# Performance work log

Hardware: AMD Instinct MI355X
Metric: run time of the kernel (lower is better)

The kernel has to match this reference:

```python
import jax, jax.numpy as jnp
import numpy as np
import math

D_MODEL, N_HEADS, D_K, D_V = 512, 2, 64, 64
C_CLIP = 10.0
MASK_FILL = -10.0

def setup_inputs() -> dict:
    key = jax.random.key(0)
    ks = jax.random.split(key, 12)
    B, Lq, Lk = 4, 2048, 2048
    s = 1.0 / math.sqrt(D_MODEL)
    return {
        "Q": jax.random.normal(ks[0], (B, Lq, D_MODEL), jnp.float32),
        "K": jax.random.normal(ks[1], (B, Lk, D_MODEL), jnp.float32),
        "V": jax.random.normal(ks[2], (B, Lk, D_MODEL), jnp.float32),
        "mask": jax.random.randint(ks[3], (B, Lk), 0, 2) > 0,
        "Wq": jax.random.normal(ks[4], (D_MODEL, N_HEADS * D_K), jnp.float32) * s,
        "bq": jnp.zeros((N_HEADS * D_K,), jnp.float32),
        "Wk": jax.random.normal(ks[5], (D_MODEL, N_HEADS * D_K), jnp.float32) * s,
        "bk": jnp.zeros((N_HEADS * D_K,), jnp.float32),
        "Wv": jax.random.normal(ks[6], (D_MODEL, N_HEADS * D_V), jnp.float32) * s,
        "bv": jnp.zeros((N_HEADS * D_V,), jnp.float32),
        "Wo": jax.random.normal(ks[7], (N_HEADS * D_V, D_MODEL), jnp.float32) * s,
        "bo": jnp.zeros((D_MODEL,), jnp.float32),
    }

def reference(Q, K, V, mask, Wq, bq, Wk, bk, Wv, bv, Wo, bo):
    B, Lq, _ = Q.shape
    Lk = K.shape[1]
    # project and split heads: [B, h, L, d]
    q = (Q @ Wq + bq).reshape(B, Lq, N_HEADS, D_K).transpose(0, 2, 1, 3)
    k = (K @ Wk + bk).reshape(B, Lk, N_HEADS, D_K).transpose(0, 2, 1, 3)
    v = (V @ Wv + bv).reshape(B, Lk, N_HEADS, D_V).transpose(0, 2, 1, 3)
    scores = jnp.einsum("bhqd,bhkd->bhqk", q, k) / jnp.sqrt(jnp.float32(D_K))
    scores = jnp.tanh(scores) * C_CLIP
    scores = jnp.where(mask[:, None, None, :], MASK_FILL, scores)
    attn = jax.nn.log_softmax(scores, axis=-1)  # NOTE: log-softmax used directly as weights
    out = jnp.einsum("bhqk,bhkd->bhqd", attn, v)
    out = out.transpose(0, 2, 1, 3).reshape(B, Lq, N_HEADS * D_V)
    out = out @ Wo + bo
    return (out, attn)
```

## Files before the change

kernel.cpp:

```cpp
#include <hip/hip_runtime.h>

typedef __attribute__((ext_vector_type(8))) short short8;
typedef __attribute__((ext_vector_type(4))) float f32x4;

#define DEVI static __device__ __forceinline__

constexpr int NB   = 4;
constexpr int NH   = 2;
constexpr int SEQ  = 2048;
constexpr int DM   = 512;
constexpr int DKV  = 64;
constexpr int HDIM = 128;

DEVI unsigned short f2bf(float f) {
    union { float f; unsigned u; } v; v.f = f;
    unsigned r = v.u + 0x7FFFu + ((v.u >> 16) & 1u);
    return (unsigned short)(r >> 16);
}
DEVI float bf2f(unsigned short s) {
    union { unsigned u; float f; } v; v.u = ((unsigned)s) << 16; return v.f;
}
DEVI void async16(const void* g, void* l) {
    __builtin_amdgcn_global_load_lds(
        (const __attribute__((address_space(1))) unsigned int*)g,
        (__attribute__((address_space(3))) unsigned int*)l, 16, 0, 0);
}

__global__ __launch_bounds__(256) void k_prep(
    const float* __restrict__ Wq, const float* __restrict__ Wk,
    const float* __restrict__ Wv, const float* __restrict__ Wo,
    unsigned short* __restrict__ Wqt, unsigned short* __restrict__ Wkt,
    unsigned short* __restrict__ Wvt, unsigned short* __restrict__ Wot) {
    int id = blockIdx.x * 256 + threadIdx.x;
    int which = id >> 16;
    int rem = id & 65535;
    if (which < 3) {
        const float* W = which == 0 ? Wq : (which == 1 ? Wk : Wv);
        unsigned short* Wt = which == 0 ? Wqt : (which == 1 ? Wkt : Wvt);
        int n = rem >> 9, k = rem & 511;
        Wt[rem] = f2bf(W[k * HDIM + n]);
    } else {
        int n = rem >> 7, k = rem & 127;
        Wot[rem] = f2bf(Wo[k * DM + n]);
    }
}

__global__ __launch_bounds__(256) void k_proj(
    const float* __restrict__ Qg, const float* __restrict__ Kg, const float* __restrict__ Vg,
    const unsigned short* __restrict__ Wqt, const unsigned short* __restrict__ Wkt,
    const unsigned short* __restrict__ Wvt,
    const float* __restrict__ bq, const float* __restrict__ bk, const float* __restrict__ bv,
    unsigned short* __restrict__ qs, unsigned short* __restrict__ kb,
    unsigned short* __restrict__ vt) {
    __shared__ unsigned short lA[64 * 64];
    __shared__ unsigned short lB[128 * 64];

    const int y = blockIdx.y;
    const float* X = y == 0 ? Qg : (y == 1 ? Kg : Vg);
    const unsigned short* Wt = y == 0 ? Wqt : (y == 1 ? Wkt : Wvt);
    const float* bias = y == 0 ? bq : (y == 1 ? bk : bv);
    const float scal = y == 0 ? 0.125f : 1.0f;
    const int row0 = blockIdx.x * 64;
    const int tid = threadIdx.x, lane = tid & 63, wv = tid >> 6;
    const int l16 = lane & 15, lq4 = lane >> 4;
    const int wr = wv >> 1, wc = wv & 1;

    f32x4 acc[2][4];
    #pragma unroll
    for (int i = 0; i < 2; ++i)
        #pragma unroll
        for (int j = 0; j < 4; ++j) acc[i][j] = f32x4{0.f, 0.f, 0.f, 0.f};

    const int arow = tid >> 2, ac0 = (tid & 3) * 16;

    for (int kc = 0; kc < 8; ++kc) {
        {
            const float* src = X + (size_t)(row0 + arow) * DM + kc * 64 + ac0;
            #pragma unroll
            for (int i = 0; i < 4; ++i) {
                float4 v = *(const float4*)(src + 4 * i);
                unsigned p0 = (unsigned)f2bf(v.x) | ((unsigned)f2bf(v.y) << 16);
                unsigned p1 = (unsigned)f2bf(v.z) | ((unsigned)f2bf(v.w) << 16);
                int slot = ((tid & 3) * 2 + (i >> 1)) ^ (arow & 7);
                char* d = (char*)lA + arow * 128 + slot * 16 + (i & 1) * 8;
                *(unsigned*)d = p0;
                *(unsigned*)(d + 4) = p1;
            }
        }
        #pragma unroll
        for (int c = 0; c < 4; ++c) {
            int chunk = wv * 4 + c;
            int n = chunk * 8 + (lane >> 3);
            int gslot = (lane & 7) ^ (n & 7);
            const void* g = (const char*)Wt + ((size_t)n * DM + kc * 64) * 2 + gslot * 16;
            void* l = (char*)lB + chunk * 1024 + lane * 16;
            async16(g, l);
        }
        __syncthreads();

        #pragma unroll
        for (int ks = 0; ks < 2; ++ks) {
            short8 a[2], b[4];
            #pragma unroll
            for (int mt = 0; mt < 2; ++mt) {
                int m = wr * 32 + mt * 16 + l16;
                unsigned ao = (unsigned)(m * 128 + ks * 64 + lq4 * 16) ^ ((unsigned)(m & 7) << 4);
                a[mt] = *(const short8*)((const char*)lA + ao);
            }
            #pragma unroll
            for (int nt = 0; nt < 4; ++nt) {
                int n = wc * 64 + nt * 16 + l16;
                unsigned bo2 = (unsigned)(n * 128 + ks * 64 + lq4 * 16) ^ ((unsigned)(n & 7) << 4);
                b[nt] = *(const short8*)((const char*)lB + bo2);
            }
            #pragma unroll
            for (int mt = 0; mt < 2; ++mt)
                #pragma unroll
                for (int nt = 0; nt < 4; ++nt)
                    acc[mt][nt] = __builtin_amdgcn_mfma_f32_16x16x32_bf16(
                        a[mt], b[nt], acc[mt][nt], 0, 0, 0);
        }
        __syncthreads();
    }

    if (y < 2) {
        unsigned short* dstp = (y == 0) ? qs : kb;
        #pragma unroll
        for (int mt = 0; mt < 2; ++mt)
            #pragma unroll
            for (int nt = 0; nt < 4; ++nt) {
                int col = wc * 64 + nt * 16 + l16;
                float bb = bias[col];
                int h = col >> 6, d = col & 63;
                #pragma unroll
                for (int r = 0; r < 4; ++r) {
                    int row = row0 + wr * 32 + mt * 16 + lq4 * 4 + r;
                    int b = row >> 11, pos = row & 2047;
                    float val = (acc[mt][nt][r] + bb) * scal;
                    dstp[((size_t)(b * NH + h) * SEQ + pos) * DKV + d] = f2bf(val);
                }
            }
    } else {
        #pragma unroll
        for (int mt = 0; mt < 2; ++mt)
            #pragma unroll
            for (int nt = 0; nt < 4; ++nt) {
                int col = wc * 64 + nt * 16 + l16;
                float bb = bias[col];
                #pragma unroll
                for (int r = 0; r < 4; ++r) {
                    int mrow = wr * 32 + mt * 16 + lq4 * 4 + r;
                    lB[col * 64 + mrow] = f2bf(acc[mt][nt][r] + bb);
                }
            }
        __syncthreads();
        int c = tid >> 1, mp = (tid & 1) * 32;
        int b = row0 >> 11, kpos0 = row0 & 2047;
        int h = c >> 6, d = c & 63;
        unsigned short* dst = vt + ((size_t)(b * NH + h) * DKV + d) * SEQ + kpos0 + mp;
        const unsigned short* srcl = &lB[c * 64 + mp];
        #pragma unroll
        for (int i = 0; i < 4; ++i)
            *(uint4*)(dst + 8 * i) = *(const uint4*)(srcl + 8 * i);
    }
}

__global__ __launch_bounds__(512) void k_fused(
    const unsigned short* __restrict__ qs, const unsigned short* __restrict__ kb,
    const unsigned short* __restrict__ vt, const int* __restrict__ maskg,
    float* __restrict__ attnG, unsigned short* __restrict__ outh) {
    __shared__ unsigned short sAttn[32 * 2048];
    __shared__ float lsum[4][32];
    __shared__ float lL[32];

    const int wg = blockIdx.x;
    const int swz = (wg & 7) * 64 + (wg >> 3);
    const int bh = swz >> 6;
    const int qt = swz & 63;
    const int qbase = qt * 32;
    const int b = bh >> 1, h = bh & 1;
    const int tid = threadIdx.x, lane = tid & 63, wv = tid >> 6;
    const int l16 = lane & 15, lq4 = lane >> 4;
    const int wr = wv >> 2, wc = wv & 3;

    const unsigned short* qrow =
        qs + ((size_t)bh * SEQ + qbase + wr * 16 + l16) * DKV + lq4 * 8;
    short8 aq0 = *(const short8*)qrow;
    short8 aq1 = *(const short8*)(qrow + 32);

    const unsigned short* kfrag =
        kb + ((size_t)bh * SEQ + wc * 16 + l16) * DKV + lq4 * 8;
    const int* mrow = maskg + b * SEQ + wc * 16 + l16;

    const int srow_q = wr * 16 + lq4 * 4;
    const int cbase = wc * 16 + l16;

    float sums[4] = {0.f, 0.f, 0.f, 0.f};

    #pragma unroll 2
    for (int kt = 0; kt < 32; ++kt) {
        short8 b0 = *(const short8*)(kfrag + (size_t)kt * 4096);
        short8 b1 = *(const short8*)(kfrag + (size_t)kt * 4096 + 32);
        int mv = mrow[kt * 64];
        f32x4 acc = f32x4{0.f, 0.f, 0.f, 0.f};
        acc = __builtin_amdgcn_mfma_f32_16x16x32_bf16(aq0, b0, acc, 0, 0, 0);
        acc = __builtin_amdgcn_mfma_f32_16x16x32_bf16(aq1, b1, acc, 0, 0, 0);
        int col = kt * 64 + cbase;
        #pragma unroll
        for (int r = 0; r < 4; ++r) {
            float x = acc[r];
            float e2 = __expf(2.f * x);
            float s10 = 10.f - 20.f * __builtin_amdgcn_rcpf(1.f + e2);
            float s = mv ? -10.f : s10;
            sums[r] += __expf(s);
            int row = srow_q + r;
            unsigned bo = (unsigned)(row * 4096 + col * 2) ^ ((unsigned)(row & 7) << 4);
            *(unsigned short*)((char*)sAttn + bo) = f2bf(s);
        }
    }

    #pragma unroll
    for (int r = 0; r < 4; ++r) {
        float v = sums[r];
        v += __shfl_xor(v, 1); v += __shfl_xor(v, 2);
        v += __shfl_xor(v, 4); v += __shfl_xor(v, 8);
        if (l16 == 0) lsum[wc][srow_q + r] = v;
    }
    __syncthreads();
    if (tid < 32)
        lL[tid] = __logf(lsum[0][tid] + lsum[1][tid] + lsum[2][tid] + lsum[3][tid]);
    __syncthreads();

    {
        const int row = tid >> 4;
        const int cb = (tid & 15) * 8;
        const float Lv = lL[row];
        float* gdst = attnG + ((size_t)bh * SEQ + qbase + row) * SEQ;
        const unsigned rbase = (unsigned)(row * 4096);
        const unsigned rxor = (unsigned)(row & 7) << 4;
        #pragma unroll
        for (int j = 0; j < 16; ++j) {
            int c = cb + j * 128;
            unsigned bo = (rbase + (unsigned)(c * 2)) ^ rxor;
            short8 v = *(const short8*)((const char*)sAttn + bo);
            float fv[8];
            #pragma unroll
            for (int t = 0; t < 8; ++t) fv[t] = bf2f((unsigned short)v[t]) - Lv;
            float4 fa, fb;
            fa.x = fv[0]; fa.y = fv[1]; fa.z = fv[2]; fa.w = fv[3];
            fb.x = fv[4]; fb.y = fv[5]; fb.z = fv[6]; fb.w = fv[7];
            *(float4*)(gdst + c) = fa;
            *(float4*)(gdst + c + 4) = fb;
            short8 w;
            #pragma unroll
            for (int t = 0; t < 8; ++t) w[t] = (short)f2bf(fv[t]);
            *(short8*)((char*)sAttn + bo) = w;
        }
    }
    __syncthreads();

    const unsigned short* vfrag =
        vt + ((size_t)bh * DKV + wc * 16 + l16) * SEQ + lq4 * 8;
    const int arow = wr * 16 + l16;
    const unsigned abase = (unsigned)(arow * 4096);
    const unsigned axor = (unsigned)(arow & 7) << 4;
    f32x4 o = f32x4{0.f, 0.f, 0.f, 0.f};
    #pragma unroll 4
    for (int ks = 0; ks < 64; ++ks) {
        short8 af = *(const short8*)((const char*)sAttn +
                                     ((abase + (unsigned)(ks * 64 + lq4 * 16)) ^ axor));
        short8 vf = *(const short8*)(vfrag + ks * 32);
        o = __builtin_amdgcn_mfma_f32_16x16x32_bf16(af, vf, o, 0, 0, 0);
    }

    #pragma unroll
    for (int r = 0; r < 4; ++r) {
        size_t orow = (size_t)b * SEQ + qbase + wr * 16 + lq4 * 4 + r;
        outh[orow * HDIM + h * DKV + wc * 16 + l16] = f2bf(o[r]);
    }
}

__global__ __launch_bounds__(256) void k_oproj(
    const unsigned short* __restrict__ outh, const unsigned short* __restrict__ Wot,
    const float* __restrict__ bo, float* __restrict__ outG) {
    __shared__ unsigned short lA2[128 * 128];
    __shared__ unsigned short lB2[128 * 128];
    const int row0 = blockIdx.x * 128, col0 = blockIdx.y * 128;
    const int tid = threadIdx.x, lane = tid & 63, wv = tid >> 6;
    const int l16 = lane & 15, lq4 = lane >> 4;
    const int wr = wv >> 1, wc = wv & 1;

    #pragma unroll
    for (int c = 0; c < 8; ++c) {
        int chunk = wv * 8 + c;
        int row = chunk * 4 + (lane >> 4);
        int gslot = (lane & 15) ^ (row & 7);
        async16((const char*)outh + ((size_t)(row0 + row)) * 256 + gslot * 16,
                (char*)lA2 + chunk * 1024 + lane * 16);
    }
    #pragma unroll
    for (int c = 0; c < 8; ++c) {
        int chunk = wv * 8 + c;
        int row = chunk * 4 + (lane >> 4);
        int gslot = (lane & 15) ^ (row & 7);
        async16((const char*)Wot + ((size_t)(col0 + row)) * 256 + gslot * 16,
                (char*)lB2 + chunk * 1024 + lane * 16);
    }
    __syncthreads();

    f32x4 acc[4][4];
    #pragma unroll
    for (int mt = 0; mt < 4; ++mt)
        #pragma unroll
        for (int nt = 0; nt < 4; ++nt) acc[mt][nt] = f32x4{0.f, 0.f, 0.f, 0.f};

    #pragma unroll
    for (int ks = 0; ks < 4; ++ks) {
        short8 a[4], bfr[4];
        #pragma unroll
        for (int mt = 0; mt < 4; ++mt) {
            int m = wr * 64 + mt * 16 + l16;
            unsigned ao = (unsigned)(m * 256 + ks * 64 + lq4 * 16) ^ ((unsigned)(m & 7) << 4);
            a[mt] = *(const short8*)((const char*)lA2 + ao);
        }
        #pragma unroll
        for (int nt = 0; nt < 4; ++nt) {
            int n = wc * 64 + nt * 16 + l16;
            unsigned bo2 = (unsigned)(n * 256 + ks * 64 + lq4 * 16) ^ ((unsigned)(n & 7) << 4);
            bfr[nt] = *(const short8*)((const char*)lB2 + bo2);
        }
        #pragma unroll
        for (int mt = 0; mt < 4; ++mt)
            #pragma unroll
            for (int nt = 0; nt < 4; ++nt)
                acc[mt][nt] = __builtin_amdgcn_mfma_f32_16x16x32_bf16(
                    a[mt], bfr[nt], acc[mt][nt], 0, 0, 0);
    }

    #pragma unroll
    for (int nt = 0; nt < 4; ++nt) {
        int col = col0 + wc * 64 + nt * 16 + l16;
        float bb = bo[col];
        #pragma unroll
        for (int mt = 0; mt < 4; ++mt)
            #pragma unroll
            for (int r = 0; r < 4; ++r) {
                int row = row0 + wr * 64 + mt * 16 + lq4 * 4 + r;
                outG[(size_t)row * DM + col] = acc[mt][nt][r] + bb;
            }
    }
}

extern "C" void kernel_launch(void* const* d_in, const int* in_sizes, int n_in,
                              void* d_out, int out_size, void* d_ws, size_t ws_size,
                              hipStream_t stream) {
    (void)in_sizes; (void)n_in; (void)out_size; (void)ws_size;
    const float* Qg = (const float*)d_in[0];
    const float* Kg = (const float*)d_in[1];
    const float* Vg = (const float*)d_in[2];
    const int*   maskg = (const int*)d_in[3];
    const float* Wq = (const float*)d_in[4];
    const float* bq = (const float*)d_in[5];
    const float* Wk = (const float*)d_in[6];
    const float* bk = (const float*)d_in[7];
    const float* Wv = (const float*)d_in[8];
    const float* bv = (const float*)d_in[9];
    const float* Wo = (const float*)d_in[10];
    const float* bo = (const float*)d_in[11];

    char* ws = (char*)d_ws;
    unsigned short* qs   = (unsigned short*)(ws);
    unsigned short* kb   = (unsigned short*)(ws + (4  << 20));
    unsigned short* vt   = (unsigned short*)(ws + (8  << 20));
    unsigned short* outh = (unsigned short*)(ws + (28 << 20));
    unsigned short* Wqt  = (unsigned short*)(ws + (30 << 20) + 262144);
    unsigned short* Wkt  = (unsigned short*)((char*)Wqt + 131072);
    unsigned short* Wvt  = (unsigned short*)((char*)Wkt + 131072);
    unsigned short* Wot  = (unsigned short*)((char*)Wvt + 131072);

    float* outG  = (float*)d_out;
    float* attnG = outG + (size_t)NB * SEQ * DM;

    hipLaunchKernelGGL(k_prep, dim3(1024), dim3(256), 0, stream,
                       Wq, Wk, Wv, Wo, Wqt, Wkt, Wvt, Wot);
    hipLaunchKernelGGL(k_proj, dim3(128, 3), dim3(256), 0, stream,
                       Qg, Kg, Vg, Wqt, Wkt, Wvt, bq, bk, bv, qs, kb, vt);
    hipLaunchKernelGGL(k_fused, dim3(512), dim3(512), 0, stream,
                       qs, kb, vt, maskg, attnG, outh);
    hipLaunchKernelGGL(k_oproj, dim3(64, 4), dim3(256), 0, stream, outh, Wot, bo, outG);
}
```

Before: 281.8 us.

## Factor log-softmax out of PV, double threads in fused attention, shrink projection tiles

The PV product now uses the raw clipped scores, and subtracts logsumexp times a precomputed column-sum of V, computed by a new small k_vsum kernel. This removes the rewrite of normalized bf16 attention into shared memory and one barrier. The fused kernel goes from 512 to 1024 threads, splits the PV reduction over two key halves combined through shared memory, and software-prefetches K and V fragments. Folding 2x into the Q scale lets the tanh skip a multiply. The projection kernel moves to 32-row tiles to launch more blocks. Risks include bf16 precision in the factored form and higher register pressure at 1024 threads.

```diff
diff --git a/kernel.cpp b/kernel.cpp
--- a/kernel.cpp
+++ b/kernel.cpp
@@ -52,40 +52,39 @@
     const float* __restrict__ bq, const float* __restrict__ bk, const float* __restrict__ bv,
     unsigned short* __restrict__ qs, unsigned short* __restrict__ kb,
     unsigned short* __restrict__ vt) {
-    __shared__ unsigned short lA[64 * 64];
+    __shared__ unsigned short lA[32 * 64];
     __shared__ unsigned short lB[128 * 64];
 
     const int y = blockIdx.y;
     const float* X = y == 0 ? Qg : (y == 1 ? Kg : Vg);
     const unsigned short* Wt = y == 0 ? Wqt : (y == 1 ? Wkt : Wvt);
     const float* bias = y == 0 ? bq : (y == 1 ? bk : bv);
-    const float scal = y == 0 ? 0.125f : 1.0f;
-    const int row0 = blockIdx.x * 64;
+    const float scal = y == 0 ? 0.25f : 1.0f;
+    const int row0 = blockIdx.x * 32;
     const int tid = threadIdx.x, lane = tid & 63, wv = tid >> 6;
     const int l16 = lane & 15, lq4 = lane >> 4;
-    const int wr = wv >> 1, wc = wv & 1;
-
-    f32x4 acc[2][4];
+    const int wc = wv;
+
+    f32x4 acc[2][2];
     #pragma unroll
     for (int i = 0; i < 2; ++i)
         #pragma unroll
-        for (int j = 0; j < 4; ++j) acc[i][j] = f32x4{0.f, 0.f, 0.f, 0.f};
-
-    const int arow = tid >> 2, ac0 = (tid & 3) * 16;
+        for (int j = 0; j < 2; ++j) acc[i][j] = f32x4{0.f, 0.f, 0.f, 0.f};
+
+    const int arow = tid >> 3, ac0 = (tid & 7) * 8;
 
     for (int kc = 0; kc < 8; ++kc) {
         {
             const float* src = X + (size_t)(row0 + arow) * DM + kc * 64 + ac0;
-            #pragma unroll
-            for (int i = 0; i < 4; ++i) {
-                float4 v = *(const float4*)(src + 4 * i);
-                unsigned p0 = (unsigned)f2bf(v.x) | ((unsigned)f2bf(v.y) << 16);
-                unsigned p1 = (unsigned)f2bf(v.z) | ((unsigned)f2bf(v.w) << 16);
-                int slot = ((tid & 3) * 2 + (i >> 1)) ^ (arow & 7);
-                char* d = (char*)lA + arow * 128 + slot * 16 + (i & 1) * 8;
-                *(unsigned*)d = p0;
-                *(unsigned*)(d + 4) = p1;
-            }
+            float4 v0 = *(const float4*)src;
+            float4 v1 = *(const float4*)(src + 4);
+            unsigned q0 = (unsigned)f2bf(v0.x) | ((unsigned)f2bf(v0.y) << 16);
+            unsigned q1 = (unsigned)f2bf(v0.z) | ((unsigned)f2bf(v0.w) << 16);
+            unsigned q2 = (unsigned)f2bf(v1.x) | ((unsigned)f2bf(v1.y) << 16);
+            unsigned q3 = (unsigned)f2bf(v1.z) | ((unsigned)f2bf(v1.w) << 16);
+            int slot = (tid & 7) ^ (arow & 7);
+            unsigned* d = (unsigned*)((char*)lA + arow * 128 + slot * 16);
+            d[0] = q0; d[1] = q1; d[2] = q2; d[3] = q3;
         }
         #pragma unroll
         for (int c = 0; c < 4; ++c) {
@@ -100,23 +99,23 @@
 
         #pragma unroll
         for (int ks = 0; ks < 2; ++ks) {
-            short8 a[2], b[4];
+            short8 a[2], b[2];
             #pragma unroll
             for (int mt = 0; mt < 2; ++mt) {
-                int m = wr * 32 + mt * 16 + l16;
+                int m = mt * 16 + l16;
                 unsigned ao = (unsigned)(m * 128 + ks * 64 + lq4 * 16) ^ ((unsigned)(m & 7) << 4);
                 a[mt] = *(const short8*)((const char*)lA + ao);
             }
             #pragma unroll
-            for (int nt = 0; nt < 4; ++nt) {
-                int n = wc * 64 + nt * 16 + l16;
+            for (int nt = 0; nt < 2; ++nt) {
+                int n = wc * 32 + nt * 16 + l16;
                 unsigned bo2 = (unsigned)(n * 128 + ks * 64 + lq4 * 16) ^ ((unsigned)(n & 7) << 4);
                 b[nt] = *(const short8*)((const char*)lB + bo2);
             }
             #pragma unroll
             for (int mt = 0; mt < 2; ++mt)
                 #pragma unroll
-                for (int nt = 0; nt < 4; ++nt)
+                for (int nt = 0; nt < 2; ++nt)
                     acc[mt][nt] = __builtin_amdgcn_mfma_f32_16x16x32_bf16(
                         a[mt], b[nt], acc[mt][nt], 0, 0, 0);
         }
@@ -128,13 +127,13 @@
         #pragma unroll
         for (int mt = 0; mt < 2; ++mt)
             #pragma unroll
-            for (int nt = 0; nt < 4; ++nt) {
-                int col = wc * 64 + nt * 16 + l16;
+            for (int nt = 0; nt < 2; ++nt) {
+                int col = wc * 32 + nt * 16 + l16;
                 float bb = bias[col];
                 int h = col >> 6, d = col & 63;
                 #pragma unroll
                 for (int r = 0; r < 4; ++r) {
-                    int row = row0 + wr * 32 + mt * 16 + lq4 * 4 + r;
+                    int row = row0 + mt * 16 + lq4 * 4 + r;
                     int b = row >> 11, pos = row & 2047;
                     float val = (acc[mt][nt][r] + bb) * scal;
                     dstp[((size_t)(b * NH + h) * SEQ + pos) * DKV + d] = f2bf(val);
@@ -144,34 +143,51 @@
         #pragma unroll
         for (int mt = 0; mt < 2; ++mt)
             #pragma unroll
-            for (int nt = 0; nt < 4; ++nt) {
-                int col = wc * 64 + nt * 16 + l16;
+            for (int nt = 0; nt < 2; ++nt) {
+                int col = wc * 32 + nt * 16 + l16;
                 float bb = bias[col];
                 #pragma unroll
                 for (int r = 0; r < 4; ++r) {
-                    int mrow = wr * 32 + mt * 16 + lq4 * 4 + r;
-                    lB[col * 64 + mrow] = f2bf(acc[mt][nt][r] + bb);
+                    int mrow = mt * 16 + lq4 * 4 + r;
+                    lB[col * 32 + mrow] = f2bf(acc[mt][nt][r] + bb);
                 }
             }
         __syncthreads();
-        int c = tid >> 1, mp = (tid & 1) * 32;
+        int c = tid >> 1, mp = (tid & 1) * 16;
         int b = row0 >> 11, kpos0 = row0 & 2047;
         int h = c >> 6, d = c & 63;
         unsigned short* dst = vt + ((size_t)(b * NH + h) * DKV + d) * SEQ + kpos0 + mp;
-        const unsigned short* srcl = &lB[c * 64 + mp];
-        #pragma unroll
-        for (int i = 0; i < 4; ++i)
-            *(uint4*)(dst + 8 * i) = *(const uint4*)(srcl + 8 * i);
-    }
-}
-
-__global__ __launch_bounds__(512) void k_fused(
+        const unsigned short* srcl = &lB[c * 32 + mp];
+        *(uint4*)dst = *(const uint4*)srcl;
+        *(uint4*)(dst + 8) = *(const uint4*)(srcl + 8);
+    }
+}
+
+__global__ __launch_bounds__(512) void k_vsum(const unsigned short* __restrict__ vt,
+                                              float* __restrict__ vs) {
+    int bh = blockIdx.x, tid = threadIdx.x;
+    int d = tid >> 3, oct = tid & 7;
+    const unsigned short* src = vt + ((size_t)bh * DKV + d) * SEQ + oct * 256;
+    float s = 0.f;
+    #pragma unroll 4
+    for (int i = 0; i < 32; ++i) {
+        short8 v = *(const short8*)(src + i * 8);
+        #pragma unroll
+        for (int t = 0; t < 8; ++t) s += bf2f((unsigned short)v[t]);
+    }
+    s += __shfl_xor(s, 1); s += __shfl_xor(s, 2); s += __shfl_xor(s, 4);
+    if (oct == 0) vs[bh * DKV + d] = s;
+}
+
+__global__ __launch_bounds__(1024, 4) void k_fused(
     const unsigned short* __restrict__ qs, const unsigned short* __restrict__ kb,
     const unsigned short* __restrict__ vt, const int* __restrict__ maskg,
-    float* __restrict__ attnG, unsigned short* __restrict__ outh) {
+    const float* __restrict__ vsumG, float* __restrict__ attnG,
+    unsigned short* __restrict__ outh) {
     __shared__ unsigned short sAttn[32 * 2048];
-    __shared__ float lsum[4][32];
+    __shared__ float lsum[8][32];
     __shared__ float lL[32];
+    __shared__ float pvbuf[8][16][16];
 
     const int wg = blockIdx.x;
     const int swz = (wg & 7) * 64 + (wg >> 3);
@@ -181,7 +197,7 @@
     const int b = bh >> 1, h = bh & 1;
     const int tid = threadIdx.x, lane = tid & 63, wv = tid >> 6;
     const int l16 = lane & 15, lq4 = lane >> 4;
-    const int wr = wv >> 2, wc = wv & 3;
+    const int wr = wv >> 3, wc8 = wv & 7;
 
     const unsigned short* qrow =
         qs + ((size_t)bh * SEQ + qbase + wr * 16 + l16) * DKV + lq4 * 8;
@@ -189,34 +205,38 @@
     short8 aq1 = *(const short8*)(qrow + 32);
 
     const unsigned short* kfrag =
-        kb + ((size_t)bh * SEQ + wc * 16 + l16) * DKV + lq4 * 8;
-    const int* mrow = maskg + b * SEQ + wc * 16 + l16;
-
-    const int srow_q = wr * 16 + lq4 * 4;
-    const int cbase = wc * 16 + l16;
+        kb + ((size_t)bh * SEQ + wc8 * 16 + l16) * DKV + lq4 * 8;
+    const int* mrow = maskg + b * SEQ + wc8 * 16 + l16;
+
+    const int srow = wr * 16 + lq4 * 4;
+    const int cb = wc8 * 16 + l16;
 
     float sums[4] = {0.f, 0.f, 0.f, 0.f};
 
-    #pragma unroll 2
-    for (int kt = 0; kt < 32; ++kt) {
-        short8 b0 = *(const short8*)(kfrag + (size_t)kt * 4096);
-        short8 b1 = *(const short8*)(kfrag + (size_t)kt * 4096 + 32);
-        int mv = mrow[kt * 64];
+    short8 b0 = *(const short8*)kfrag;
+    short8 b1 = *(const short8*)(kfrag + 32);
+    int mv = mrow[0];
+    for (int kt = 0; kt < 16; ++kt) {
+        int nx = (kt + 1) & 15;
+        short8 nb0 = *(const short8*)(kfrag + (size_t)nx * 8192);
+        short8 nb1 = *(const short8*)(kfrag + (size_t)nx * 8192 + 32);
+        int nmv = mrow[nx * 128];
         f32x4 acc = f32x4{0.f, 0.f, 0.f, 0.f};
         acc = __builtin_amdgcn_mfma_f32_16x16x32_bf16(aq0, b0, acc, 0, 0, 0);
         acc = __builtin_amdgcn_mfma_f32_16x16x32_bf16(aq1, b1, acc, 0, 0, 0);
-        int col = kt * 64 + cbase;
+        int col = kt * 128 + cb;
         #pragma unroll
         for (int r = 0; r < 4; ++r) {
             float x = acc[r];
-            float e2 = __expf(2.f * x);
+            float e2 = __expf(x);
             float s10 = 10.f - 20.f * __builtin_amdgcn_rcpf(1.f + e2);
             float s = mv ? -10.f : s10;
             sums[r] += __expf(s);
-            int row = srow_q + r;
+            int row = srow + r;
             unsigned bo = (unsigned)(row * 4096 + col * 2) ^ ((unsigned)(row & 7) << 4);
             *(unsigned short*)((char*)sAttn + bo) = f2bf(s);
         }
+        b0 = nb0; b1 = nb1; mv = nmv;
     }
 
     #pragma unroll
@@ -224,59 +244,71 @@
         float v = sums[r];
         v += __shfl_xor(v, 1); v += __shfl_xor(v, 2);
         v += __shfl_xor(v, 4); v += __shfl_xor(v, 8);
-        if (l16 == 0) lsum[wc][srow_q + r] = v;
+        if (l16 == 0) lsum[wc8][srow + r] = v;
     }
     __syncthreads();
-    if (tid < 32)
-        lL[tid] = __logf(lsum[0][tid] + lsum[1][tid] + lsum[2][tid] + lsum[3][tid]);
+    if (tid < 32) {
+        float t = lsum[0][tid] + lsum[1][tid] + lsum[2][tid] + lsum[3][tid] +
+                  lsum[4][tid] + lsum[5][tid] + lsum[6][tid] + lsum[7][tid];
+        lL[tid] = __logf(t);
+    }
     __syncthreads();
 
     {
-        const int row = tid >> 4;
-        const int cb = (tid & 15) * 8;
+        const int row = tid >> 5;
+        const int cb2 = (tid & 31) * 8;
         const float Lv = lL[row];
         float* gdst = attnG + ((size_t)bh * SEQ + qbase + row) * SEQ;
         const unsigned rbase = (unsigned)(row * 4096);
         const unsigned rxor = (unsigned)(row & 7) << 4;
         #pragma unroll
-        for (int j = 0; j < 16; ++j) {
-            int c = cb + j * 128;
+        for (int j = 0; j < 8; ++j) {
+            int c = cb2 + j * 256;
             unsigned bo = (rbase + (unsigned)(c * 2)) ^ rxor;
             short8 v = *(const short8*)((const char*)sAttn + bo);
-            float fv[8];
-            #pragma unroll
-            for (int t = 0; t < 8; ++t) fv[t] = bf2f((unsigned short)v[t]) - Lv;
             float4 fa, fb;
-            fa.x = fv[0]; fa.y = fv[1]; fa.z = fv[2]; fa.w = fv[3];
-            fb.x = fv[4]; fb.y = fv[5]; fb.z = fv[6]; fb.w = fv[7];
+            fa.x = bf2f((unsigned short)v[0]) - Lv;
+            fa.y = bf2f((unsigned short)v[1]) - Lv;
+            fa.z = bf2f((unsigned short)v[2]) - Lv;
+            fa.w = bf2f((unsigned short)v[3]) - Lv;
+            fb.x = bf2f((unsigned short)v[4]) - Lv;
+            fb.y = bf2f((unsigned short)v[5]) - Lv;
+            fb.z = bf2f((unsigned short)v[6]) - Lv;
+            fb.w = bf2f((unsigned short)v[7]) - Lv;
             *(float4*)(gdst + c) = fa;
             *(float4*)(gdst + c + 4) = fb;
-            short8 w;
-            #pragma unroll
-            for (int t = 0; t < 8; ++t) w[t] = (short)f2bf(fv[t]);
-            *(short8*)((char*)sAttn + bo) = w;
-        }
-    }
-    __syncthreads();
-
+        }
+    }
+
+    const int kh = wv >> 3, dg = (wv >> 1) & 3, pr = wv & 1;
     const unsigned short* vfrag =
-        vt + ((size_t)bh * DKV + wc * 16 + l16) * SEQ + lq4 * 8;
-    const int arow = wr * 16 + l16;
-    const unsigned abase = (unsigned)(arow * 4096);
+        vt + ((size_t)bh * DKV + dg * 16 + l16) * SEQ + kh * 1024 + lq4 * 8;
+    const int arow = pr * 16 + l16;
+    const unsigned abase = (unsigned)(arow * 4096 + kh * 2048 + lq4 * 16);
     const unsigned axor = (unsigned)(arow & 7) << 4;
     f32x4 o = f32x4{0.f, 0.f, 0.f, 0.f};
-    #pragma unroll 4
-    for (int ks = 0; ks < 64; ++ks) {
+    short8 vf = *(const short8*)vfrag;
+    for (int ks = 0; ks < 32; ++ks) {
+        short8 nvf = *(const short8*)(vfrag + ((ks + 1) & 31) * 32);
         short8 af = *(const short8*)((const char*)sAttn +
-                                     ((abase + (unsigned)(ks * 64 + lq4 * 16)) ^ axor));
-        short8 vf = *(const short8*)(vfrag + ks * 32);
+                                     ((abase + (unsigned)(ks * 64)) ^ axor));
         o = __builtin_amdgcn_mfma_f32_16x16x32_bf16(af, vf, o, 0, 0, 0);
-    }
-
-    #pragma unroll
-    for (int r = 0; r < 4; ++r) {
-        size_t orow = (size_t)b * SEQ + qbase + wr * 16 + lq4 * 4 + r;
-        outh[orow * HDIM + h * DKV + wc * 16 + l16] = f2bf(o[r]);
+        vf = nvf;
+    }
+    if (kh) {
+        #pragma unroll
+        for (int r = 0; r < 4; ++r) pvbuf[dg * 2 + pr][lq4 * 4 + r][l16] = o[r];
+    }
+    __syncthreads();
+    if (!kh) {
+        const float vs = vsumG[bh * DKV + dg * 16 + l16];
+        #pragma unroll
+        for (int r = 0; r < 4; ++r) {
+            int qr = pr * 16 + lq4 * 4 + r;
+            float val = o[r] + pvbuf[dg * 2 + pr][lq4 * 4 + r][l16] - lL[qr] * vs;
+            outh[((size_t)b * SEQ + qbase + qr) * HDIM + h * DKV + dg * 16 + l16] =
+                f2bf(val);
+        }
     }
 }
 
@@ -373,6 +405,7 @@
     unsigned short* kb   = (unsigned short*)(ws + (4  << 20));
     unsigned short* vt   = (unsigned short*)(ws + (8  << 20));
     unsigned short* outh = (unsigned short*)(ws + (28 << 20));
+    float*          vsum = (float*)(ws + (30 << 20));
     unsigned short* Wqt  = (unsigned short*)(ws + (30 << 20) + 262144);
     unsigned short* Wkt  = (unsigned short*)((char*)Wqt + 131072);
     unsigned short* Wvt  = (unsigned short*)((char*)Wkt + 131072);
@@ -383,9 +416,10 @@
 
     hipLaunchKernelGGL(k_prep, dim3(1024), dim3(256), 0, stream,
                        Wq, Wk, Wv, Wo, Wqt, Wkt, Wvt, Wot);
-    hipLaunchKernelGGL(k_proj, dim3(128, 3), dim3(256), 0, stream,
+    hipLaunchKernelGGL(k_proj, dim3(256, 3), dim3(256), 0, stream,
                        Qg, Kg, Vg, Wqt, Wkt, Wvt, bq, bk, bv, qs, kb, vt);
-    hipLaunchKernelGGL(k_fused, dim3(512), dim3(512), 0, stream,
-                       qs, kb, vt, maskg, attnG, outh);
+    hipLaunchKernelGGL(k_vsum, dim3(8), dim3(512), 0, stream, vt, vsum);
+    hipLaunchKernelGGL(k_fused, dim3(512), dim3(1024), 0, stream,
+                       qs, kb, vt, maskg, vsum, attnG, outh);
     hipLaunchKernelGGL(k_oproj, dim3(64, 4), dim3(256), 0, stream, outh, Wot, bo, outG);
 }
```

Result: no change. 283.7 us (+0.7%).

## Restructure attention kernel to 16-row tiles with split-K PV and LDS transpose prep

Applied to the files above, without the earlier changes.

The attention kernel now uses 1024-thread blocks over 16 query rows. Scores stay in registers until the log-sum-exp is known, so normalized log-probabilities are written to LDS once and then streamed to global memory. The PV product is split across 16 waves along K, with partial results reduced through shared memory. Separately, weight prep uses an LDS-tiled transpose for coalesced access, k_proj drops its LDS XOR swizzle (which risks bank conflicts), and the workspace layout is compacted. Doubling the block count means each K/V tile is reloaded more often, and the larger blocks limit occupancy to one per CU.

```diff
diff --git a/kernel.cpp b/kernel.cpp
--- a/kernel.cpp
+++ b/kernel.cpp
@@ -20,6 +20,9 @@
 DEVI float bf2f(unsigned short s) {
     union { unsigned u; float f; } v; v.u = ((unsigned)s) << 16; return v.f;
 }
+DEVI unsigned pk2(float a, float b) {
+    return (unsigned)f2bf(a) | ((unsigned)f2bf(b) << 16);
+}
 DEVI void async16(const void* g, void* l) {
     __builtin_amdgcn_global_load_lds(
         (const __attribute__((address_space(1))) unsigned int*)g,
@@ -31,18 +34,37 @@
     const float* __restrict__ Wv, const float* __restrict__ Wo,
     unsigned short* __restrict__ Wqt, unsigned short* __restrict__ Wkt,
     unsigned short* __restrict__ Wvt, unsigned short* __restrict__ Wot) {
-    int id = blockIdx.x * 256 + threadIdx.x;
-    int which = id >> 16;
-    int rem = id & 65535;
-    if (which < 3) {
-        const float* W = which == 0 ? Wq : (which == 1 ? Wk : Wv);
-        unsigned short* Wt = which == 0 ? Wqt : (which == 1 ? Wkt : Wvt);
-        int n = rem >> 9, k = rem & 511;
-        Wt[rem] = f2bf(W[k * HDIM + n]);
+    __shared__ unsigned short T[64][72];
+    const int bid = blockIdx.x, tid = threadIdx.x;
+    const float* src; unsigned short* dst; int ss, ds, k0, n0;
+    if (bid < 48) {
+        int m = bid >> 4, t16 = bid & 15;
+        src = m == 0 ? Wq : (m == 1 ? Wk : Wv);
+        dst = m == 0 ? Wqt : (m == 1 ? Wkt : Wvt);
+        ss = 128; ds = 512;
+        k0 = (t16 >> 1) * 64; n0 = (t16 & 1) * 64;
     } else {
-        int n = rem >> 7, k = rem & 127;
-        Wot[rem] = f2bf(Wo[k * DM + n]);
-    }
+        int t16 = bid - 48;
+        src = Wo; dst = Wot; ss = 512; ds = 128;
+        k0 = (t16 >> 3) * 64; n0 = (t16 & 7) * 64;
+    }
+    const int kk = tid >> 4, nn4 = (tid & 15) * 4;
+    #pragma unroll
+    for (int i = 0; i < 4; ++i) {
+        float4 v = *(const float4*)(src + (size_t)(k0 + kk + i * 16) * ss + n0 + nn4);
+        T[kk + i * 16][nn4]     = f2bf(v.x);
+        T[kk + i * 16][nn4 + 1] = f2bf(v.y);
+        T[kk + i * 16][nn4 + 2] = f2bf(v.z);
+        T[kk + i * 16][nn4 + 3] = f2bf(v.w);
+    }
+    __syncthreads();
+    const int nn = tid >> 2, kc = (tid & 3) * 16;
+    unsigned short tmp[16];
+    #pragma unroll
+    for (int i = 0; i < 16; ++i) tmp[i] = T[kc + i][nn];
+    unsigned short* o = dst + (size_t)(n0 + nn) * ds + k0 + kc;
+    *(uint4*)o       = *(uint4*)tmp;
+    *(uint4*)(o + 8) = *(uint4*)(tmp + 8);
 }
 
 __global__ __launch_bounds__(256) void k_proj(
@@ -76,23 +98,22 @@
     for (int kc = 0; kc < 8; ++kc) {
         {
             const float* src = X + (size_t)(row0 + arow) * DM + kc * 64 + ac0;
+            unsigned short* dst = &lA[arow * 64 + ac0];
             #pragma unroll
             for (int i = 0; i < 4; ++i) {
                 float4 v = *(const float4*)(src + 4 * i);
                 unsigned p0 = (unsigned)f2bf(v.x) | ((unsigned)f2bf(v.y) << 16);
                 unsigned p1 = (unsigned)f2bf(v.z) | ((unsigned)f2bf(v.w) << 16);
-                int slot = ((tid & 3) * 2 + (i >> 1)) ^ (arow & 7);
-                char* d = (char*)lA + arow * 128 + slot * 16 + (i & 1) * 8;
-                *(unsigned*)d = p0;
-                *(unsigned*)(d + 4) = p1;
+                *(unsigned*)(dst + 4 * i) = p0;
+                *(unsigned*)(dst + 4 * i + 2) = p1;
             }
         }
         #pragma unroll
         for (int c = 0; c < 4; ++c) {
             int chunk = wv * 4 + c;
             int n = chunk * 8 + (lane >> 3);
-            int gslot = (lane & 7) ^ (n & 7);
-            const void* g = (const char*)Wt + ((size_t)n * DM + kc * 64) * 2 + gslot * 16;
+            int kpart = (lane & 7) * 8;
+            const void* g = (const char*)Wt + ((size_t)n * DM + kc * 64 + kpart) * 2;
             void* l = (char*)lB + chunk * 1024 + lane * 16;
             async16(g, l);
         }
@@ -104,14 +125,12 @@
             #pragma unroll
             for (int mt = 0; mt < 2; ++mt) {
                 int m = wr * 32 + mt * 16 + l16;
-                unsigned ao = (unsigned)(m * 128 + ks * 64 + lq4 * 16) ^ ((unsigned)(m & 7) << 4);
-                a[mt] = *(const short8*)((const char*)lA + ao);
+                a[mt] = *(const short8*)&lA[m * 64 + ks * 32 + lq4 * 8];
             }
             #pragma unroll
             for (int nt = 0; nt < 4; ++nt) {
                 int n = wc * 64 + nt * 16 + l16;
-                unsigned bo2 = (unsigned)(n * 128 + ks * 64 + lq4 * 16) ^ ((unsigned)(n & 7) << 4);
-                b[nt] = *(const short8*)((const char*)lB + bo2);
+                b[nt] = *(const short8*)&lB[n * 64 + ks * 32 + lq4 * 8];
             }
             #pragma unroll
             for (int mt = 0; mt < 2; ++mt)
@@ -165,47 +184,43 @@
     }
 }
 
-__global__ __launch_bounds__(512) void k_fused(
+__global__ __launch_bounds__(1024, 1) void k_attn(
     const unsigned short* __restrict__ qs, const unsigned short* __restrict__ kb,
     const unsigned short* __restrict__ vt, const int* __restrict__ maskg,
     float* __restrict__ attnG, unsigned short* __restrict__ outh) {
-    __shared__ unsigned short sAttn[32 * 2048];
-    __shared__ float lsum[4][32];
-    __shared__ float lL[32];
-
-    const int wg = blockIdx.x;
-    const int swz = (wg & 7) * 64 + (wg >> 3);
-    const int bh = swz >> 6;
-    const int qt = swz & 63;
-    const int qbase = qt * 32;
+    __shared__ unsigned short lAttn[16 * 2048];
+    __shared__ float oBuf[16][16][64];
+    __shared__ float lsum[16][16];
+    __shared__ float lL[16];
+
+    const int bx = blockIdx.x;
+    const int bh = bx & 7;
+    const int qt = bx >> 3;
+    const int qbase = qt * 16;
     const int b = bh >> 1, h = bh & 1;
     const int tid = threadIdx.x, lane = tid & 63, wv = tid >> 6;
     const int l16 = lane & 15, lq4 = lane >> 4;
-    const int wr = wv >> 2, wc = wv & 3;
 
     const unsigned short* qrow =
-        qs + ((size_t)bh * SEQ + qbase + wr * 16 + l16) * DKV + lq4 * 8;
-    short8 aq0 = *(const short8*)qrow;
-    short8 aq1 = *(const short8*)(qrow + 32);
-
-    const unsigned short* kfrag =
-        kb + ((size_t)bh * SEQ + wc * 16 + l16) * DKV + lq4 * 8;
-    const int* mrow = maskg + b * SEQ + wc * 16 + l16;
-
-    const int srow_q = wr * 16 + lq4 * 4;
-    const int cbase = wc * 16 + l16;
-
+        qs + ((size_t)bh * SEQ + qbase + l16) * DKV + lq4 * 8;
+    const short8 aq0 = *(const short8*)qrow;
+    const short8 aq1 = *(const short8*)(qrow + 32);
+
+    const unsigned short* kB = kb + (size_t)bh * SEQ * DKV;
+    const int* mB = maskg + b * SEQ;
+
+    f32x4 sraw[8];
     float sums[4] = {0.f, 0.f, 0.f, 0.f};
-
-    #pragma unroll 2
-    for (int kt = 0; kt < 32; ++kt) {
-        short8 b0 = *(const short8*)(kfrag + (size_t)kt * 4096);
-        short8 b1 = *(const short8*)(kfrag + (size_t)kt * 4096 + 32);
-        int mv = mrow[kt * 64];
+    #pragma unroll
+    for (int j = 0; j < 8; ++j) {
+        int n = wv * 128 + j * 16 + l16;
+        const unsigned short* p = kB + (size_t)n * DKV + lq4 * 8;
+        short8 b0 = *(const short8*)p;
+        short8 b1 = *(const short8*)(p + 32);
+        int mv = mB[n];
         f32x4 acc = f32x4{0.f, 0.f, 0.f, 0.f};
         acc = __builtin_amdgcn_mfma_f32_16x16x32_bf16(aq0, b0, acc, 0, 0, 0);
         acc = __builtin_amdgcn_mfma_f32_16x16x32_bf16(aq1, b1, acc, 0, 0, 0);
-        int col = kt * 64 + cbase;
         #pragma unroll
         for (int r = 0; r < 4; ++r) {
             float x = acc[r];
@@ -213,9 +228,7 @@
             float s10 = 10.f - 20.f * __builtin_amdgcn_rcpf(1.f + e2);
             float s = mv ? -10.f : s10;
             sums[r] += __expf(s);
-            int row = srow_q + r;
-            unsigned bo = (unsigned)(row * 4096 + col * 2) ^ ((unsigned)(row & 7) << 4);
-            *(unsigned short*)((char*)sAttn + bo) = f2bf(s);
+            sraw[j][r] = s;
         }
     }
 
@@ -224,59 +237,88 @@
         float v = sums[r];
         v += __shfl_xor(v, 1); v += __shfl_xor(v, 2);
         v += __shfl_xor(v, 4); v += __shfl_xor(v, 8);
-        if (l16 == 0) lsum[wc][srow_q + r] = v;
-    }
-    __syncthreads();
-    if (tid < 32)
-        lL[tid] = __logf(lsum[0][tid] + lsum[1][tid] + lsum[2][tid] + lsum[3][tid]);
+        if (l16 == 0) lsum[wv][lq4 * 4 + r] = v;
+    }
+    __syncthreads();
+    if (tid < 16) {
+        float t = 0.f;
+        #pragma unroll
+        for (int w = 0; w < 16; ++w) t += lsum[w][tid];
+        lL[tid] = __logf(t);
+    }
     __syncthreads();
 
     {
-        const int row = tid >> 4;
-        const int cb = (tid & 15) * 8;
-        const float Lv = lL[row];
-        float* gdst = attnG + ((size_t)bh * SEQ + qbase + row) * SEQ;
+        float Lr[4];
+        #pragma unroll
+        for (int r = 0; r < 4; ++r) Lr[r] = lL[lq4 * 4 + r];
+        #pragma unroll
+        for (int j = 0; j < 8; ++j) {
+            int col = wv * 128 + j * 16 + l16;
+            #pragma unroll
+            for (int r = 0; r < 4; ++r) {
+                int row = lq4 * 4 + r;
+                float a = sraw[j][r] - Lr[r];
+                unsigned bo = (unsigned)(row * 4096 + col * 2) ^ ((unsigned)(row & 7) << 4);
+                *(unsigned short*)((char*)lAttn + bo) = f2bf(a);
+            }
+        }
+    }
+    __syncthreads();
+
+    {
+        const int row = tid >> 6;
+        const int c0 = (tid & 63) * 8;
+        float* drow = attnG + ((size_t)bh * SEQ + qbase + row) * SEQ;
         const unsigned rbase = (unsigned)(row * 4096);
         const unsigned rxor = (unsigned)(row & 7) << 4;
         #pragma unroll
-        for (int j = 0; j < 16; ++j) {
-            int c = cb + j * 128;
-            unsigned bo = (rbase + (unsigned)(c * 2)) ^ rxor;
-            short8 v = *(const short8*)((const char*)sAttn + bo);
-            float fv[8];
-            #pragma unroll
-            for (int t = 0; t < 8; ++t) fv[t] = bf2f((unsigned short)v[t]) - Lv;
+        for (int j = 0; j < 4; ++j) {
+            int c = c0 + j * 512;
+            short8 v = *(const short8*)((const char*)lAttn + ((rbase + (unsigned)(c * 2)) ^ rxor));
             float4 fa, fb;
-            fa.x = fv[0]; fa.y = fv[1]; fa.z = fv[2]; fa.w = fv[3];
-            fb.x = fv[4]; fb.y = fv[5]; fb.z = fv[6]; fb.w = fv[7];
-            *(float4*)(gdst + c) = fa;
-            *(float4*)(gdst + c + 4) = fb;
-            short8 w;
-            #pragma unroll
-            for (int t = 0; t < 8; ++t) w[t] = (short)f2bf(fv[t]);
-            *(short8*)((char*)sAttn + bo) = w;
-        }
-    }
-    __syncthreads();
-
-    const unsigned short* vfrag =
-        vt + ((size_t)bh * DKV + wc * 16 + l16) * SEQ + lq4 * 8;
-    const int arow = wr * 16 + l16;
-    const unsigned abase = (unsigned)(arow * 4096);
-    const unsigned axor = (unsigned)(arow & 7) << 4;
-    f32x4 o = f32x4{0.f, 0.f, 0.f, 0.f};
-    #pragma unroll 4
-    for (int ks = 0; ks < 64; ++ks) {
-        short8 af = *(const short8*)((const char*)sAttn +
-                                     ((abase + (unsigned)(ks * 64 + lq4 * 16)) ^ axor));
-        short8 vf = *(const short8*)(vfrag + ks * 32);
-        o = __builtin_amdgcn_mfma_f32_16x16x32_bf16(af, vf, o, 0, 0, 0);
-    }
-
-    #pragma unroll
-    for (int r = 0; r < 4; ++r) {
-        size_t orow = (size_t)b * SEQ + qbase + wr * 16 + lq4 * 4 + r;
-        outh[orow * HDIM + h * DKV + wc * 16 + l16] = f2bf(o[r]);
+            fa.x = bf2f((unsigned short)v[0]); fa.y = bf2f((unsigned short)v[1]);
+            fa.z = bf2f((unsigned short)v[2]); fa.w = bf2f((unsigned short)v[3]);
+            fb.x = bf2f((unsigned short)v[4]); fb.y = bf2f((unsigned short)v[5]);
+            fb.z = bf2f((unsigned short)v[6]); fb.w = bf2f((unsigned short)v[7]);
+            *(float4*)(drow + c) = fa;
+            *(float4*)(drow + c + 4) = fb;
+        }
+    }
+
+    {
+        const int k0 = wv * 128;
+        f32x4 o[4];
+        #pragma unroll
+        for (int nt = 0; nt < 4; ++nt) o[nt] = f32x4{0.f, 0.f, 0.f, 0.f};
+        const unsigned abase = (unsigned)(l16 * 4096 + k0 * 2);
+        const unsigned axor = (unsigned)(l16 & 7) << 4;
+        #pragma unroll
+        for (int ks = 0; ks < 4; ++ks) {
+            short8 af = *(const short8*)((const char*)lAttn +
+                          ((abase + (unsigned)(ks * 64 + lq4 * 16)) ^ axor));
+            #pragma unroll
+            for (int nt = 0; nt < 4; ++nt) {
+                const unsigned short* vp =
+                    vt + ((size_t)bh * DKV + nt * 16 + l16) * SEQ + k0 + ks * 32 + lq4 * 8;
+                short8 vf = *(const short8*)vp;
+                o[nt] = __builtin_amdgcn_mfma_f32_16x16x32_bf16(af, vf, o[nt], 0, 0, 0);
+            }
+        }
+        #pragma unroll
+        for (int nt = 0; nt < 4; ++nt)
+            #pragma unroll
+            for (int r = 0; r < 4; ++r)
+                oBuf[wv][lq4 * 4 + r][nt * 16 + l16] = o[nt][r];
+    }
+    __syncthreads();
+
+    {
+        const int row = tid >> 6, d = tid & 63;
+        float s = 0.f;
+        #pragma unroll
+        for (int w = 0; w < 16; ++w) s += oBuf[w][row][d];
+        outh[((size_t)b * SEQ + qbase + row) * HDIM + h * DKV + d] = f2bf(s);
     }
 }
 
@@ -372,8 +414,8 @@
     unsigned short* qs   = (unsigned short*)(ws);
     unsigned short* kb   = (unsigned short*)(ws + (4  << 20));
     unsigned short* vt   = (unsigned short*)(ws + (8  << 20));
-    unsigned short* outh = (unsigned short*)(ws + (28 << 20));
-    unsigned short* Wqt  = (unsigned short*)(ws + (30 << 20) + 262144);
+    unsigned short* outh = (unsigned short*)(ws + (12 << 20));
+    unsigned short* Wqt  = (unsigned short*)(ws + (16 << 20));
     unsigned short* Wkt  = (unsigned short*)((char*)Wqt + 131072);
     unsigned short* Wvt  = (unsigned short*)((char*)Wkt + 131072);
     unsigned short* Wot  = (unsigned short*)((char*)Wvt + 131072);
@@ -381,11 +423,11 @@
     float* outG  = (float*)d_out;
     float* attnG = outG + (size_t)NB * SEQ * DM;
 
-    hipLaunchKernelGGL(k_prep, dim3(1024), dim3(256), 0, stream,
+    hipLaunchKernelGGL(k_prep, dim3(64), dim3(256), 0, stream,
                        Wq, Wk, Wv, Wo, Wqt, Wkt, Wvt, Wot);
     hipLaunchKernelGGL(k_proj, dim3(128, 3), dim3(256), 0, stream,
                        Qg, Kg, Vg, Wqt, Wkt, Wvt, bq, bk, bv, qs, kb, vt);
-    hipLaunchKernelGGL(k_fused, dim3(512), dim3(512), 0, stream,
+    hipLaunchKernelGGL(k_attn, dim3(1024), dim3(1024), 0, stream,
                        qs, kb, vt, maskg, attnG, outh);
     hipLaunchKernelGGL(k_oproj, dim3(64, 4), dim3(256), 0, stream, outh, Wot, bo, outG);
 }
```

Result: slower. 287.6 us (+2.1%).
